# Kernel tuning notes

Hardware: AMD Instinct MI355X
Metric: run time of the kernel (lower is better)

## Reference

```python
import jax, jax.numpy as jnp
import numpy as np

B, S, D = 8, 1024, 1024
E, M, K = 8, 4096, 2
GROUP = 1024
CAP = int(np.ceil(GROUP * K / E))  # 256 tokens per expert per group


def setup_inputs() -> dict:
    key = jax.random.key(0)
    ks = jax.random.split(key, 4)
    x = jax.random.normal(ks[0], (B, S, D), dtype=jnp.float32)
    w_router = jax.random.normal(ks[1], (D, E), dtype=jnp.float32) * 0.02
    w1 = jax.random.normal(ks[2], (E, D, M), dtype=jnp.float32) * (1.0 / np.sqrt(D))
    b1 = jnp.zeros((E, M), dtype=jnp.float32)
    w2 = jax.random.normal(ks[3], (E, M, D), dtype=jnp.float32) * (1.0 / np.sqrt(M))
    b2 = jnp.zeros((E, D), dtype=jnp.float32)
    return {"x": x, "w_router": w_router, "w1": w1, "b1": b1, "w2": w2, "b2": b2}


def _moe_forward(x, w_router, w1, b1, w2, b2):
    # Group tokens: [G, GROUP, D]
    xg = x.reshape(-1, GROUP, D)
    G = xg.shape[0]
    # Router: gates over experts per token.
    logits = jnp.einsum('gsd,de->gse', xg, w_router)
    gates = jax.nn.softmax(logits, axis=-1)  # [G, S, E]
    topk_vals, topk_idx = jax.lax.top_k(gates, K)  # [G, S, K]
    oh = jax.nn.one_hot(topk_idx, E, dtype=xg.dtype)  # [G, S, K, E]

    # Position in each expert's buffer: choice-0 of all tokens has priority
    # over choice-1 (standard top-k MoE priority ordering).
    prev = jnp.zeros((G, 1, E), dtype=xg.dtype)
    dispatch = jnp.zeros((G, GROUP, E, CAP), dtype=xg.dtype)
    combine = jnp.zeros((G, GROUP, E, CAP), dtype=xg.dtype)
    for k in range(K):
        ohk = oh[:, :, k, :]                                  # [G, S, E]
        csum = jnp.cumsum(ohk, axis=1) - ohk + prev           # slots used before this token
        pos_k = jnp.sum(csum * ohk, axis=-1)                  # [G, S]
        keep = (pos_k < CAP).astype(xg.dtype)
        pos_oh = jax.nn.one_hot(pos_k, CAP, dtype=xg.dtype)   # [G, S, C]
        d_k = ohk[:, :, :, None] * pos_oh[:, :, None, :] * keep[:, :, None, None]
        dispatch = dispatch + d_k
        combine = combine + topk_vals[:, :, k, None, None] * d_k
        prev = prev + jnp.sum(ohk, axis=1, keepdims=True)

    # Dispatch tokens into per-expert buffers: [E, G, C, D]
    xe = jnp.einsum('gsec,gsd->egcd', dispatch, xg)
    # Per-expert MLP (gelu, approximate=True as in flax Dense MlpBlock).
    h = jax.nn.gelu(jnp.einsum('egcd,edm->egcm', xe, w1) + b1[:, None, None, :])
    ye = jnp.einsum('egcm,emd->egcd', h, w2) + b2[:, None, None, :]
    # Combine back to tokens, weighted by gates.
    out = jnp.einsum('gsec,egcd->gsd', combine, ye)
    out = out.reshape(B, S, D)

    # Importance auxiliary metric (squared coefficient of variation of gate mass).
    imp = jnp.sum(gates, axis=1)  # [G, E]
    aux = jnp.mean((jnp.std(imp, axis=-1) / jnp.mean(imp, axis=-1)) ** 2)
    return out, aux


def reference(x, w_router, w1, b1, w2, b2):
    return _moe_forward(x, w_router, w1, b1, w2, b2)
```

## Files before the change

### kernel.cpp

```cpp
#include <hip/hip_runtime.h>

#define D_DIM 1024
#define E_EXP 8
#define M_DIM 4096
#define N_GRP 8
#define GRP_SZ 1024
#define CAPACITY 256
#define N_TOK (N_GRP * GRP_SZ)
#define SLOT_ROWS (E_EXP * N_GRP * CAPACITY)
#define ROWS_PER_E (N_GRP * CAPACITY)

typedef _Float16 half8_t __attribute__((ext_vector_type(8)));
typedef float f32x4_t __attribute__((ext_vector_type(4)));

__device__ __forceinline__ void async_copy16(void* lds, const void* gptr) {
  __builtin_amdgcn_global_load_lds(
      (__attribute__((address_space(1))) void*)(void*)(const_cast<void*>(gptr)),
      (__attribute__((address_space(3))) void*)lds,
      16, 0, 0);
}

__device__ __forceinline__ float fast_gelu(float v) {
  float w2 = 1.5957691216057308f * (v + 0.044715f * v * v * v);
  float ex = __expf(w2);
  float t = 1.0f - 2.0f * __builtin_amdgcn_rcpf(1.0f + ex);
  return 0.5f * v * (1.0f + t);
}

__global__ __launch_bounds__(256)
void router_kernel(const float* __restrict__ x, const float* __restrict__ wr,
                   float* __restrict__ gates, int* __restrict__ tk_idx,
                   float* __restrict__ tk_val) {
  __shared__ __attribute__((aligned(16))) float wrT[E_EXP * D_DIM];
  const int tid = threadIdx.x;
  for (int i = tid; i < E_EXP * D_DIM; i += 256) {
    int d = i >> 3, e = i & 7;
    wrT[e * D_DIM + d] = wr[i];
  }
  __syncthreads();
  const int wv = tid >> 6, lane = tid & 63;
  const int token = blockIdx.x * 4 + wv;
  const float4* xr = (const float4*)(x + (size_t)token * D_DIM);
  float lg[8] = {0.f, 0.f, 0.f, 0.f, 0.f, 0.f, 0.f, 0.f};
#pragma unroll
  for (int it = 0; it < 4; it++) {
    float4 v = xr[it * 64 + lane];
#pragma unroll
    for (int e = 0; e < 8; e++) {
      float4 w = *(const float4*)&wrT[e * D_DIM + (it * 64 + lane) * 4];
      lg[e] += v.x * w.x + v.y * w.y + v.z * w.z + v.w * w.w;
    }
  }
#pragma unroll
  for (int off = 32; off > 0; off >>= 1) {
#pragma unroll
    for (int e = 0; e < 8; e++) lg[e] += __shfl_xor(lg[e], off, 64);
  }
  if (lane == 0) {
    float mx = lg[0];
#pragma unroll
    for (int e = 1; e < 8; e++) mx = fmaxf(mx, lg[e]);
    float s = 0.f, g[8];
#pragma unroll
    for (int e = 0; e < 8; e++) { g[e] = expf(lg[e] - mx); s += g[e]; }
    float inv = 1.0f / s;
#pragma unroll
    for (int e = 0; e < 8; e++) { g[e] *= inv; gates[(size_t)token * 8 + e] = g[e]; }
    int i0 = 0; float v0 = g[0];
    for (int e = 1; e < 8; e++) if (g[e] > v0) { v0 = g[e]; i0 = e; }
    int i1 = -1; float v1 = -1.f;
    for (int e = 0; e < 8; e++) if (e != i0 && g[e] > v1) { v1 = g[e]; i1 = e; }
    tk_idx[token * 2 + 0] = i0; tk_idx[token * 2 + 1] = i1;
    tk_val[token * 2 + 0] = v0; tk_val[token * 2 + 1] = v1;
  }
}

__global__ void scan_kernel(const int* __restrict__ tk_idx,
                            int* __restrict__ slot_src,
                            int* __restrict__ assign_row) {
  const int g = blockIdx.x;
  const int lane = threadIdx.x;
  const unsigned long long below = (1ull << lane) - 1ull;
  int ev[32];
#pragma unroll
  for (int k = 0; k < 2; k++)
#pragma unroll
    for (int ch = 0; ch < 16; ch++)
      ev[k * 16 + ch] = tk_idx[((size_t)g * GRP_SZ + ch * 64 + lane) * 2 + k];
  int cnt[8] = {0, 0, 0, 0, 0, 0, 0, 0};
#pragma unroll
  for (int k = 0; k < 2; k++) {
#pragma unroll
    for (int ch = 0; ch < 16; ch++) {
      const int s = ch * 64 + lane;
      const int e = ev[k * 16 + ch];
      int pos = 0;
#pragma unroll
      for (int ee = 0; ee < 8; ee++) {
        unsigned long long m = __ballot(e == ee);
        if (e == ee) pos = cnt[ee] + (int)__popcll(m & below);
        cnt[ee] += (int)__popcll(m);
      }
      int row = (pos < CAPACITY) ? ((e * N_GRP + g) * CAPACITY + pos) : -1;
      assign_row[((size_t)g * GRP_SZ + s) * 2 + k] = row;
      if (row >= 0) slot_src[row] = s;
    }
  }
  for (int e = 0; e < 8; e++)
    for (int c = lane; c < CAPACITY; c += 64)
      if (c >= cnt[e]) slot_src[(e * N_GRP + g) * CAPACITY + c] = -1;
}

__global__ __launch_bounds__(256)
void gather_kernel(const float* __restrict__ x, const int* __restrict__ slot_src,
                   _Float16* __restrict__ A1) {
  const int row = blockIdx.x;
  const int g = (row >> 8) & 7;
  const int t = threadIdx.x;
  const int s = slot_src[row];
  float2* dst = (float2*)(A1 + (size_t)row * D_DIM);
  if (s < 0) { dst[t] = make_float2(0.f, 0.f); return; }
  const float4 v = ((const float4*)x)[((size_t)g * GRP_SZ + s) * (D_DIM / 4) + t];
  union { _Float16 h[4]; float2 f2; } u;
  u.h[0] = (_Float16)v.x; u.h[1] = (_Float16)v.y;
  u.h[2] = (_Float16)v.z; u.h[3] = (_Float16)v.w;
  dst[t] = u.f2;
}

__global__ __launch_bounds__(256)
void transpose_both_kernel(const float* __restrict__ w1, const float* __restrict__ w2,
                           _Float16* __restrict__ w1t, _Float16* __restrict__ w2t) {
  __shared__ float tile[32][33];
  const int z = blockIdx.y;
  const float* sp;
  _Float16* dp;
  int R, C;
  if (z < 8) { sp = w1 + (size_t)z * D_DIM * M_DIM; dp = w1t + (size_t)z * D_DIM * M_DIM; R = D_DIM; C = M_DIM; }
  else       { sp = w2 + (size_t)(z - 8) * M_DIM * D_DIM; dp = w2t + (size_t)(z - 8) * M_DIM * D_DIM; R = M_DIM; C = D_DIM; }
  const int tiles_x = C >> 5;
  const int c0 = (blockIdx.x % tiles_x) * 32, r0 = (blockIdx.x / tiles_x) * 32;
  {
    const int row = threadIdx.x >> 3;
    const int cb = (threadIdx.x & 7) * 4;
    float4 v = *(const float4*)&sp[(size_t)(r0 + row) * C + c0 + cb];
    tile[row][cb + 0] = v.x; tile[row][cb + 1] = v.y;
    tile[row][cb + 2] = v.z; tile[row][cb + 3] = v.w;
  }
  __syncthreads();
  const int cl = threadIdx.x >> 3;
  const int ch = threadIdx.x & 7;
  union { _Float16 h[4]; float2 f2; } u;
#pragma unroll
  for (int k = 0; k < 4; k++) u.h[k] = (_Float16)tile[ch * 4 + k][cl];
  *(float2*)&dp[(size_t)(c0 + cl) * R + r0 + ch * 4] = u.f2;
}

template <int KDIM, int NDIM, int EPI>
__global__ __launch_bounds__(512, 2)
void gemm256_kernel(const _Float16* __restrict__ Aall,
                    const _Float16* __restrict__ BTall,
                    const float* __restrict__ biasAll,
                    void* __restrict__ CoutAll) {
  constexpr int NT = KDIM / 64;
  constexpr int NXT = ROWS_PER_E / 256;
  constexpr int NYT = NDIM / 256;
  constexpr int NB = NXT * NYT;
  static_assert(NXT == 8 && (NB % 8) == 0 && NT >= 4, "geometry");

  extern __shared__ __attribute__((aligned(16))) _Float16 smem[];
  _Float16* lA = smem;
  _Float16* lB = smem + 32768;

  const int e = blockIdx.z;
  const _Float16* A  = Aall  + (size_t)e * ROWS_PER_E * KDIM;
  const _Float16* BT = BTall + (size_t)e * NDIM * KDIM;
  const float* bias  = biasAll + (size_t)e * NDIM;

  const int bswz = (blockIdx.x & 7) * (NB >> 3) + (blockIdx.x >> 3);
  const int xt = bswz & (NXT - 1);
  const int yt = bswz >> 3;
  const int rowblk = xt * 256;
  const int colblk = yt * 256;

  const int tid = threadIdx.x;
  const int wave = tid >> 6, lane = tid & 63;
  const int wm = wave >> 2, wn = wave & 3;
  const int quad = lane >> 4, ln = lane & 15;

  const int schunk = (tid & 7) ^ ((tid >> 3) & 7);
  const int rowA = ((tid >> 3) << 1) + (schunk >> 2);
  const int colA = (schunk & 3) << 3;
  const _Float16* baseA = A  + (size_t)(rowblk + rowA) * KDIM + colA;
  const _Float16* baseB = BT + (size_t)(colblk + rowA) * KDIM + colA;
  const int ldsW = wave * 512;

  auto stage_unit = [&](int u) {
    const int tu = u >> 2;
    const int j = u & 3;
    const int ks = j >> 1;
    const int koff = tu * 64 + ks * 32;
    const int slot = ((tu & 1) * 2 + ks) * 8192 + ldsW;
    if ((j & 1) == 0) {
      const _Float16* g = baseA + koff;
      async_copy16(lA + slot, g);
      async_copy16(lA + slot + 4096, g + (size_t)128 * KDIM);
    } else {
      const _Float16* g = baseB + koff;
      async_copy16(lB + slot, g);
      async_copy16(lB + slot + 4096, g + (size_t)128 * KDIM);
    }
  };

  const int swc = (((ln & 1) << 2) | quad) ^ (ln >> 1);
  int offA[8], offB[4];
#pragma unroll
  for (int i = 0; i < 8; ++i)
    offA[i] = (wm * 64 + i * 8 + (ln >> 1)) * 64 + swc * 8;
#pragma unroll
  for (int j = 0; j < 4; ++j)
    offB[j] = (wn * 32 + j * 8 + (ln >> 1)) * 64 + swc * 8;

  f32x4_t acc[8][4] = {};

#pragma unroll
  for (int u = 0; u < 5; ++u) stage_unit(u);
  asm volatile("s_waitcnt vmcnt(6)" ::: "memory");
  __builtin_amdgcn_s_barrier();

  for (int t = 0; t < NT; ++t) {
    const int bufo = (t & 1) * 2 * 8192;
    half8_t bf[4];
#pragma unroll
    for (int p = 0; p < 4; ++p) {
      const int ks = p >> 1;
      const int ms = (p & 1) * 4;
      const _Float16* Ap = lA + bufo + ks * 8192;
      const _Float16* Bp = lB + bufo + ks * 8192;
      half8_t af[4];
#pragma unroll
      for (int i = 0; i < 4; ++i) af[i] = *(const half8_t*)&Ap[offA[ms + i]];
      if ((p & 1) == 0) {
#pragma unroll
        for (int j = 0; j < 4; ++j) bf[j] = *(const half8_t*)&Bp[offB[j]];
      }
      {
        const int u = 4 * t + p + 5;
        if (u < 4 * NT) stage_unit(u);
      }
      __builtin_amdgcn_s_barrier();
      __builtin_amdgcn_s_setprio(1);
#pragma unroll
      for (int i = 0; i < 4; ++i)
#pragma unroll
        for (int j = 0; j < 4; ++j)
          acc[ms + i][j] = __builtin_amdgcn_mfma_f32_16x16x32_f16(
              af[i], bf[j], acc[ms + i][j], 0, 0, 0);
      __builtin_amdgcn_s_setprio(0);
      if (p == 1) {
        if (t == NT - 1) asm volatile("s_waitcnt vmcnt(0)" ::: "memory");
        else             asm volatile("s_waitcnt vmcnt(6)" ::: "memory");
      } else if (p == 3) {
        if (t == NT - 2)     asm volatile("s_waitcnt vmcnt(4)" ::: "memory");
        else if (t < NT - 2) asm volatile("s_waitcnt vmcnt(6)" ::: "memory");
      }
      __builtin_amdgcn_s_barrier();
    }
  }

  __syncthreads();

  float bcol[4];
#pragma unroll
  for (int j = 0; j < 4; ++j) bcol[j] = bias[colblk + wn * 64 + j * 16 + ln];

  if constexpr (EPI == 1) {
    _Float16* Cc = (_Float16*)CoutAll + (size_t)e * ROWS_PER_E * NDIM;
    _Float16* eb = smem + wave * 1280;
#pragma unroll
    for (int i = 0; i < 8; ++i) {
#pragma unroll
      for (int j = 0; j < 4; ++j)
#pragma unroll
        for (int r = 0; r < 4; ++r)
          eb[(quad * 4 + r) * 72 + j * 16 + ln] =
              (_Float16)fast_gelu(acc[i][j][r] + bcol[j]);
#pragma unroll
      for (int q = 0; q < 2; ++q) {
        const int rl = q * 8 + (lane >> 3);
        const int ch = lane & 7;
        float4 vv = *(const float4*)&eb[rl * 72 + ch * 8];
        *(float4*)&Cc[(size_t)(rowblk + wm * 128 + i * 16 + rl) * NDIM +
                      colblk + wn * 64 + ch * 8] = vv;
      }
    }
  } else {
    float* Cc = (float*)CoutAll + (size_t)e * ROWS_PER_E * NDIM;
#pragma unroll
    for (int i = 0; i < 8; ++i)
#pragma unroll
      for (int j = 0; j < 4; ++j)
#pragma unroll
        for (int r = 0; r < 4; ++r)
          Cc[(size_t)(rowblk + wm * 128 + i * 16 + quad * 4 + r) * NDIM +
             colblk + wn * 64 + j * 16 + ln] = acc[i][j][r] + bcol[j];
  }
}

__global__ __launch_bounds__(256)
void combine_kernel(const float* __restrict__ ye, const int* __restrict__ assign_row,
                    const float* __restrict__ tk_val, float* __restrict__ out) {
  const int t = blockIdx.x;
  const int d = threadIdx.x;
  const int r0 = assign_row[t * 2 + 0];
  const int r1 = assign_row[t * 2 + 1];
  const float g0 = tk_val[t * 2 + 0];
  const float g1 = tk_val[t * 2 + 1];
  const float4* y4 = (const float4*)ye;
  float4 v = make_float4(0.f, 0.f, 0.f, 0.f);
  if (r0 >= 0) {
    float4 a = y4[(size_t)r0 * (D_DIM / 4) + d];
    v.x += g0 * a.x; v.y += g0 * a.y; v.z += g0 * a.z; v.w += g0 * a.w;
  }
  if (r1 >= 0) {
    float4 a = y4[(size_t)r1 * (D_DIM / 4) + d];
    v.x += g1 * a.x; v.y += g1 * a.y; v.z += g1 * a.z; v.w += g1 * a.w;
  }
  ((float4*)out)[(size_t)t * (D_DIM / 4) + d] = v;
}

__global__ __launch_bounds__(256)
void aux1_kernel(const float* __restrict__ gates, float* __restrict__ imp) {
  const int g = blockIdx.x >> 3, e = blockIdx.x & 7;
  const int tid = threadIdx.x, lane = tid & 63, wave = tid >> 6;
  float s = 0.f;
  for (int t = tid; t < GRP_SZ; t += 256)
    s += gates[((size_t)g * GRP_SZ + t) * 8 + e];
#pragma unroll
  for (int off = 32; off > 0; off >>= 1) s += __shfl_xor(s, off, 64);
  __shared__ float ws4[4];
  if (lane == 0) ws4[wave] = s;
  __syncthreads();
  if (tid == 0) imp[blockIdx.x] = ws4[0] + ws4[1] + ws4[2] + ws4[3];
}

__global__ void aux2_kernel(const float* __restrict__ imp, float* __restrict__ aux_out) {
  const int t = threadIdx.x;
  __shared__ float cvS[8];
  if (t < 8) {
    float mean = 0.f;
    for (int k = 0; k < 8; k++) mean += imp[t * 8 + k];
    mean *= 0.125f;
    float var = 0.f;
    for (int k = 0; k < 8; k++) { float dd = imp[t * 8 + k] - mean; var += dd * dd; }
    var *= 0.125f;
    cvS[t] = var / (mean * mean);
  }
  __syncthreads();
  if (t == 0) {
    float a = 0.f;
    for (int k = 0; k < 8; k++) a += cvS[k];
    aux_out[0] = a * 0.125f;
  }
}

extern "C" void kernel_launch(void* const* d_in, const int* in_sizes, int n_in,
                              void* d_out, int out_size, void* d_ws, size_t ws_size,
                              hipStream_t stream) {
  const float* x  = (const float*)d_in[0];
  const float* wr = (const float*)d_in[1];
  const float* w1 = (const float*)d_in[2];
  const float* b1 = (const float*)d_in[3];
  const float* w2 = (const float*)d_in[4];
  const float* b2 = (const float*)d_in[5];
  float* out = (float*)d_out;

  char* ws = (char*)d_ws;
  size_t off = 0;
  auto alloc = [&](size_t bytes) -> void* {
    void* p = ws + off;
    off += (bytes + 255) & ~(size_t)255;
    return p;
  };
  float*     gates      = (float*)alloc((size_t)N_TOK * 8 * 4);
  int*       tk_idx     = (int*)  alloc((size_t)N_TOK * 2 * 4);
  float*     tk_val     = (float*)alloc((size_t)N_TOK * 2 * 4);
  int*       assign_row = (int*)  alloc((size_t)N_TOK * 2 * 4);
  int*       slot_src   = (int*)  alloc((size_t)SLOT_ROWS * 4);
  float*     imp        = (float*)alloc(64 * 4);
  _Float16*  A1  = (_Float16*)alloc((size_t)SLOT_ROWS * D_DIM * 2);
  _Float16*  w1t = (_Float16*)alloc((size_t)E_EXP * M_DIM * D_DIM * 2);
  _Float16*  w2t = (_Float16*)alloc((size_t)E_EXP * D_DIM * M_DIM * 2);
  _Float16*  H   = (_Float16*)alloc((size_t)SLOT_ROWS * M_DIM * 2);
  float*     ye  = (float*)   alloc((size_t)SLOT_ROWS * D_DIM * 4);
  if (off > ws_size) return;

  router_kernel<<<N_TOK / 4, 256, 0, stream>>>(x, wr, gates, tk_idx, tk_val);
  scan_kernel<<<N_GRP, 64, 0, stream>>>(tk_idx, slot_src, assign_row);
  gather_kernel<<<SLOT_ROWS, 256, 0, stream>>>(x, slot_src, A1);
  transpose_both_kernel<<<dim3(4096, 16), 256, 0, stream>>>(w1, w2, w1t, w2t);
  gemm256_kernel<D_DIM, M_DIM, 1>
      <<<dim3((ROWS_PER_E / 256) * (M_DIM / 256), 1, E_EXP), 512, 131072, stream>>>(A1, w1t, b1, H);
  gemm256_kernel<M_DIM, D_DIM, 2>
      <<<dim3((ROWS_PER_E / 256) * (D_DIM / 256), 1, E_EXP), 512, 131072, stream>>>(H, w2t, b2, ye);
  combine_kernel<<<N_TOK, 256, 0, stream>>>(ye, assign_row, tk_val, out);
  aux1_kernel<<<64, 256, 0, stream>>>(gates, imp);
  aux2_kernel<<<1, 64, 0, stream>>>(imp, out + (size_t)N_TOK * D_DIM);
}
```

Before: 680.6 us.

## Software-pipeline LDS fragment loads across MFMA clusters and stage fp32 epilogue

Restructures the GEMM main loop so that the A/B fragment reads from LDS for the next MFMA cluster are issued before the current cluster runs, using ping-pong register sets. Global-to-LDS staging is interleaved with them, and sched_barriers pin the ordering. The fp32 output epilogue now stages each tile through shared memory and writes float4 rows instead of scattered scalar stores. This aims to hide LDS latency and improve store coalescing, at the cost of more registers and a more fragile waitcnt and barrier schedule.

```diff
diff --git a/kernel.cpp b/kernel.cpp
--- a/kernel.cpp
+++ b/kernel.cpp
@@ -194,13 +194,11 @@
   const _Float16* baseB = BT + (size_t)(colblk + rowA) * KDIM + colA;
   const int ldsW = wave * 512;
 
-  auto stage_unit = [&](int u) {
-    const int tu = u >> 2;
-    const int j = u & 3;
-    const int ks = j >> 1;
+  auto stage = [&](int tu, int ks, int isB) {
+    if (tu >= NT) return;
+    const int slot = ((tu & 1) * 2 + ks) * 8192 + ldsW;
     const int koff = tu * 64 + ks * 32;
-    const int slot = ((tu & 1) * 2 + ks) * 8192 + ldsW;
-    if ((j & 1) == 0) {
+    if (!isB) {
       const _Float16* g = baseA + koff;
       async_copy16(lA + slot, g);
       async_copy16(lA + slot + 4096, g + (size_t)128 * KDIM);
@@ -220,52 +218,84 @@
   for (int j = 0; j < 4; ++j)
     offB[j] = (wn * 32 + j * 8 + (ln >> 1)) * 64 + swc * 8;
 
+  half8_t afE[4], afO[4], bfE[4], bfO[4];
   f32x4_t acc[8][4] = {};
 
-#pragma unroll
-  for (int u = 0; u < 5; ++u) stage_unit(u);
-  asm volatile("s_waitcnt vmcnt(6)" ::: "memory");
+  stage(0, 0, 0); stage(0, 0, 1); stage(0, 1, 0); stage(0, 1, 1);
+  stage(1, 0, 0); stage(1, 0, 1);
+  asm volatile("s_waitcnt vmcnt(8)" ::: "memory");
   __builtin_amdgcn_s_barrier();
+#pragma unroll
+  for (int i = 0; i < 4; ++i) afE[i] = *(const half8_t*)&lA[offA[i]];
+#pragma unroll
+  for (int j = 0; j < 4; ++j) bfE[j] = *(const half8_t*)&lB[offB[j]];
+
+#define MFMA_CLUSTER(MS, AF, BF)                                               \
+  __builtin_amdgcn_s_setprio(1);                                               \
+  _Pragma("unroll")                                                            \
+  for (int i = 0; i < 4; ++i)                                                  \
+    _Pragma("unroll")                                                          \
+    for (int j = 0; j < 4; ++j)                                                \
+      acc[(MS) + i][j] = __builtin_amdgcn_mfma_f32_16x16x32_f16(               \
+          AF[i], BF[j], acc[(MS) + i][j], 0, 0, 0);                            \
+  __builtin_amdgcn_s_setprio(0);
 
   for (int t = 0; t < NT; ++t) {
-    const int bufo = (t & 1) * 2 * 8192;
-    half8_t bf[4];
-#pragma unroll
-    for (int p = 0; p < 4; ++p) {
-      const int ks = p >> 1;
-      const int ms = (p & 1) * 4;
-      const _Float16* Ap = lA + bufo + ks * 8192;
-      const _Float16* Bp = lB + bufo + ks * 8192;
-      half8_t af[4];
-#pragma unroll
-      for (int i = 0; i < 4; ++i) af[i] = *(const half8_t*)&Ap[offA[ms + i]];
-      if ((p & 1) == 0) {
-#pragma unroll
-        for (int j = 0; j < 4; ++j) bf[j] = *(const half8_t*)&Bp[offB[j]];
-      }
-      {
-        const int u = 4 * t + p + 5;
-        if (u < 4 * NT) stage_unit(u);
-      }
-      __builtin_amdgcn_s_barrier();
-      __builtin_amdgcn_s_setprio(1);
-#pragma unroll
-      for (int i = 0; i < 4; ++i)
-#pragma unroll
-        for (int j = 0; j < 4; ++j)
-          acc[ms + i][j] = __builtin_amdgcn_mfma_f32_16x16x32_f16(
-              af[i], bf[j], acc[ms + i][j], 0, 0, 0);
-      __builtin_amdgcn_s_setprio(0);
-      if (p == 1) {
-        if (t == NT - 1) asm volatile("s_waitcnt vmcnt(0)" ::: "memory");
-        else             asm volatile("s_waitcnt vmcnt(6)" ::: "memory");
-      } else if (p == 3) {
-        if (t == NT - 2)     asm volatile("s_waitcnt vmcnt(4)" ::: "memory");
-        else if (t < NT - 2) asm volatile("s_waitcnt vmcnt(6)" ::: "memory");
-      }
-      __builtin_amdgcn_s_barrier();
-    }
-  }
+    const int par = (t & 1) * 2;
+    const int parn = ((t + 1) & 1) * 2;
+    const _Float16* A0 = lA + par * 8192;
+    const _Float16* A1 = lA + (par + 1) * 8192;
+    const _Float16* B1 = lB + (par + 1) * 8192;
+    const _Float16* A0n = lA + parn * 8192;
+    const _Float16* B0n = lB + parn * 8192;
+
+#pragma unroll
+    for (int i = 0; i < 4; ++i) afO[i] = *(const half8_t*)&A0[offA[4 + i]];
+    stage(t + 1, 1, 0);
+    if (t < NT - 1) asm volatile("s_waitcnt vmcnt(6)" ::: "memory");
+    else            asm volatile("s_waitcnt vmcnt(0)" ::: "memory");
+    __builtin_amdgcn_sched_barrier(0);
+    __builtin_amdgcn_s_barrier();
+    MFMA_CLUSTER(0, afE, bfE)
+    __builtin_amdgcn_sched_barrier(0);
+    __builtin_amdgcn_s_barrier();
+
+#pragma unroll
+    for (int i = 0; i < 4; ++i) afE[i] = *(const half8_t*)&A1[offA[i]];
+#pragma unroll
+    for (int j = 0; j < 4; ++j) bfO[j] = *(const half8_t*)&B1[offB[j]];
+    stage(t + 1, 1, 1);
+    __builtin_amdgcn_sched_barrier(0);
+    __builtin_amdgcn_s_barrier();
+    MFMA_CLUSTER(4, afO, bfE)
+    __builtin_amdgcn_sched_barrier(0);
+    __builtin_amdgcn_s_barrier();
+
+#pragma unroll
+    for (int i = 0; i < 4; ++i) afO[i] = *(const half8_t*)&A1[offA[4 + i]];
+    stage(t + 2, 0, 0);
+    if (t < NT - 2)      asm volatile("s_waitcnt vmcnt(6)" ::: "memory");
+    else if (t == NT - 2) asm volatile("s_waitcnt vmcnt(4)" ::: "memory");
+    __builtin_amdgcn_sched_barrier(0);
+    __builtin_amdgcn_s_barrier();
+    MFMA_CLUSTER(0, afE, bfO)
+    __builtin_amdgcn_sched_barrier(0);
+    __builtin_amdgcn_s_barrier();
+
+    if (t < NT - 1) {
+#pragma unroll
+      for (int i = 0; i < 4; ++i) afE[i] = *(const half8_t*)&A0n[offA[i]];
+#pragma unroll
+      for (int j = 0; j < 4; ++j) bfE[j] = *(const half8_t*)&B0n[offB[j]];
+    }
+    stage(t + 2, 0, 1);
+    __builtin_amdgcn_sched_barrier(0);
+    __builtin_amdgcn_s_barrier();
+    MFMA_CLUSTER(4, afO, bfO)
+    __builtin_amdgcn_sched_barrier(0);
+    __builtin_amdgcn_s_barrier();
+  }
+#undef MFMA_CLUSTER
 
   __syncthreads();
 
@@ -295,14 +325,23 @@
     }
   } else {
     float* Cc = (float*)CoutAll + (size_t)e * ROWS_PER_E * NDIM;
-#pragma unroll
-    for (int i = 0; i < 8; ++i)
+    float* ebf = (float*)smem + wave * 1088;
+#pragma unroll
+    for (int i = 0; i < 8; ++i) {
 #pragma unroll
       for (int j = 0; j < 4; ++j)
 #pragma unroll
         for (int r = 0; r < 4; ++r)
-          Cc[(size_t)(rowblk + wm * 128 + i * 16 + quad * 4 + r) * NDIM +
-             colblk + wn * 64 + j * 16 + ln] = acc[i][j][r] + bcol[j];
+          ebf[(quad * 4 + r) * 68 + j * 16 + ln] = acc[i][j][r] + bcol[j];
+      const int rl = lane >> 2;
+      const int ch = lane & 3;
+#pragma unroll
+      for (int q = 0; q < 4; ++q) {
+        float4 vv = *(const float4*)&ebf[rl * 68 + q * 16 + ch * 4];
+        *(float4*)&Cc[(size_t)(rowblk + wm * 128 + i * 16 + rl) * NDIM +
+                      colblk + wn * 64 + q * 16 + ch * 4] = vv;
+      }
+    }
   }
 }
 
```

Result: no change. 672.5 us (-1.2%).
